# Performance work log

Hardware: AMD Instinct MI355X
Metric: run time of the kernel (lower is better)

Reference implementation:

```python
import jax, jax.numpy as jnp
import numpy as np

B, C, E, H = 4, 2048, 1024, 16
D = E // H
EPS = 1e-5

def _layernorm(x, g, b):
    mu = jnp.mean(x, axis=-1, keepdims=True)
    var = jnp.mean(jnp.square(x - mu), axis=-1, keepdims=True)
    return (x - mu) * jax.lax.rsqrt(var + EPS) * g + b

def setup_inputs() -> dict:
    key = jax.random.key(0)
    ks = jax.random.split(key, 12)
    s = 1.0 / np.sqrt(E)
    return {
        "inputs": jax.random.normal(ks[0], (B, C, E), dtype=jnp.float32),
        "Wq": jax.random.normal(ks[1], (E, E), dtype=jnp.float32) * s,
        "bq": jnp.zeros((E,), dtype=jnp.float32),
        "Wk": jax.random.normal(ks[2], (E, E), dtype=jnp.float32) * s,
        "bk": jnp.zeros((E,), dtype=jnp.float32),
        "Wv": jax.random.normal(ks[3], (E, E), dtype=jnp.float32) * s,
        "bv": jnp.zeros((E,), dtype=jnp.float32),
        "g1": jnp.ones((E,), dtype=jnp.float32),
        "beta1": jnp.zeros((E,), dtype=jnp.float32),
        "g2": jnp.ones((E,), dtype=jnp.float32),
        "beta2": jnp.zeros((E,), dtype=jnp.float32),
        "W1": jax.random.normal(ks[4], (E, 4 * E), dtype=jnp.float32) * s,
        "bm1": jnp.zeros((4 * E,), dtype=jnp.float32),
        "W2": jax.random.normal(ks[5], (4 * E, E), dtype=jnp.float32) * (1.0 / np.sqrt(4 * E)),
        "bm2": jnp.zeros((E,), dtype=jnp.float32),
    }

def reference(inputs, Wq, bq, Wk, bk, Wv, bv, g1, beta1, g2, beta2, W1, bm1, W2, bm2):
    b, c, e = inputs.shape
    normed = _layernorm(inputs, g1, beta1)
    q = (normed @ Wq + bq).reshape(b, c, H, D).transpose(0, 2, 1, 3)  # [B,H,C,D]
    k = (normed @ Wk + bk).reshape(b, c, H, D).transpose(0, 2, 1, 3)
    v = (normed @ Wv + bv).reshape(b, c, H, D).transpose(0, 2, 1, 3)
    scores = jnp.einsum('bhqd,bhkd->bhqk', q, k) / np.sqrt(D).astype(np.float32)
    causal = jnp.triu(jnp.ones((c, c), dtype=bool), k=1)  # True above diagonal
    scores = jnp.where(causal, -jnp.inf, scores)
    probs = jax.nn.softmax(scores, axis=-1)
    attn = jnp.einsum('bhqk,bhkd->bhqd', probs, v)
    attn = attn.transpose(0, 2, 1, 3).reshape(b, c, e)
    out = inputs + attn
    h = _layernorm(out, g2, beta2)
    mlp = jax.nn.relu(h @ W1 + bm1) @ W2 + bm2
    return out + mlp
```

## Files before the change

kernel.cpp:

```cpp
#include <hip/hip_runtime.h>
#include <math.h>

#define B_ 4
#define C_ 2048
#define E_ 1024
#define H_ 16
#define D_ 64
#define ROWS_ (B_*C_)

typedef __bf16 bf16x8 __attribute__((ext_vector_type(8)));
typedef float f32x4 __attribute__((ext_vector_type(4)));

__device__ __forceinline__ float b2f(unsigned short u) {
  unsigned int x = ((unsigned int)u) << 16;
  return __builtin_bit_cast(float, x);
}
__device__ __forceinline__ unsigned short f2b(float f) {
  unsigned int x = __builtin_bit_cast(unsigned int, f);
  unsigned int r = (x + 0x7FFFu + ((x >> 16) & 1u)) >> 16;
  return (unsigned short)r;
}
__device__ __forceinline__ unsigned short tob(float f) { return f2b(f); }
__device__ __forceinline__ unsigned short tob(unsigned short u) { return u; }
__device__ __forceinline__ void store_out(float* p, float v) { *p = v; }
__device__ __forceinline__ void store_out(unsigned short* p, float v) { *p = f2b(v); }

__device__ __forceinline__ void async16(const void* g, void* l) {
  __builtin_amdgcn_global_load_lds(
      (__attribute__((address_space(1))) unsigned int*)g,
      (__attribute__((address_space(3))) unsigned int*)l, 16, 0, 0);
}

template <typename InT>
__global__ __launch_bounds__(256) void transpose64(
    const InT* __restrict__ in, unsigned short* __restrict__ out,
    int s_in, int s_out, int Hz, long zs_b, long zs_h, long zs_out)
{
  __shared__ unsigned short t[64][65];
  int z = blockIdx.z;
  long ib = (long)(z / Hz) * zs_b + (long)(z % Hz) * zs_h;
  long ob = (long)z * zs_out;
  int r0 = blockIdx.y * 64, c0 = blockIdx.x * 64;
  int lane = threadIdx.x & 63, grp = threadIdx.x >> 6;
  for (int i = grp; i < 64; i += 4)
    t[i][lane] = tob(in[ib + (long)(r0 + i) * s_in + c0 + lane]);
  __syncthreads();
  for (int i = grp; i < 64; i += 4)
    out[ob + (long)(c0 + i) * s_out + r0 + lane] = t[lane][i];
}

__global__ void concat_bias(const float* __restrict__ q,
                            const float* __restrict__ k,
                            const float* __restrict__ v,
                            float* __restrict__ o)
{
  int i = blockIdx.x * 256 + threadIdx.x;
  o[i] = (i < 1024) ? q[i] : (i < 2048) ? k[i - 1024] : v[i - 2048];
}

__global__ __launch_bounds__(256) void ln_kernel(
    const float* __restrict__ xin, const unsigned short* __restrict__ addend,
    const float* __restrict__ g, const float* __restrict__ beta,
    unsigned short* __restrict__ yout, float* __restrict__ out1)
{
  int row = blockIdx.x, tid = threadIdx.x;
  size_t base = (size_t)row * E_ + tid * 4;
  float4 xa = *(const float4*)(xin + base);
  float v0 = xa.x, v1 = xa.y, v2 = xa.z, v3 = xa.w;
  if (addend) {
    ushort4 aa = *(const ushort4*)(addend + base);
    v0 += b2f(aa.x); v1 += b2f(aa.y); v2 += b2f(aa.z); v3 += b2f(aa.w);
  }
  if (out1) {
    *(float4*)(out1 + base) = make_float4(v0, v1, v2, v3);
  }
  float s = v0 + v1 + v2 + v3;
  float sq = v0*v0 + v1*v1 + v2*v2 + v3*v3;
  #pragma unroll
  for (int off = 32; off >= 1; off >>= 1) {
    s  += __shfl_xor(s, off);
    sq += __shfl_xor(sq, off);
  }
  __shared__ float red[8];
  int wid = tid >> 6;
  if ((tid & 63) == 0) { red[wid] = s; red[4 + wid] = sq; }
  __syncthreads();
  s  = red[0] + red[1] + red[2] + red[3];
  sq = red[4] + red[5] + red[6] + red[7];
  float mu = s * (1.0f / E_);
  float var = sq * (1.0f / E_) - mu * mu;
  float rs = rsqrtf(var + 1e-5f);
  float4 ga = *(const float4*)(g + tid * 4);
  float4 ba = *(const float4*)(beta + tid * 4);
  ushort4 o;
  o.x = f2b((v0 - mu) * rs * ga.x + ba.x);
  o.y = f2b((v1 - mu) * rs * ga.y + ba.y);
  o.z = f2b((v2 - mu) * rs * ga.z + ba.z);
  o.w = f2b((v3 - mu) * rs * ga.w + ba.w);
  *(ushort4*)(yout + base) = o;
}

template <typename OutT>
__global__ __launch_bounds__(256) void gemm_bt(
    const unsigned short* __restrict__ A, const unsigned short* __restrict__ Bt,
    const float* __restrict__ bias, const float* __restrict__ resid,
    OutT* __restrict__ Co, int M, int N, int K, int lda, int ldb,
    int relu, size_t zs)
{
  __shared__ __align__(16) unsigned short As[128 * 64];
  __shared__ __align__(16) unsigned short Bs[128 * 64];
  int tid = threadIdx.x, lane = tid & 63, wid = tid >> 6;
  int lane15 = lane & 15, quad = lane >> 4;

  int i = blockIdx.x;
  int xcd = i & 7, s = i >> 3;
  int bn = s >> 3;
  int bm = xcd * 8 + (s & 7);
  size_t koff = (size_t)blockIdx.z * K;
  Co += (size_t)blockIdx.z * zs;

  int m_lo = (wid & 1) * 64, n_lo = (wid >> 1) * 64;

  f32x4 acc[4][4];
  #pragma unroll
  for (int a = 0; a < 4; ++a)
    #pragma unroll
    for (int bb = 0; bb < 4; ++bb) acc[a][bb] = 0.0f;

  int sr = tid >> 3, sc = tid & 7;
  int scs = (sc ^ (sr & 7)) * 8;
  const unsigned short* Ag = A + koff + (size_t)(bm * 128 + sr) * lda + scs;
  const unsigned short* Bg = Bt + koff + (size_t)(bn * 128 + sr) * ldb + scs;
  unsigned short* Al = &As[wid * 512];
  unsigned short* Bl = &Bs[wid * 512];
  int sw15 = lane15 & 7;

  for (int k0 = 0; k0 < K; k0 += 64) {
    async16(Ag,                     Al);
    async16(Ag + (size_t)32 * lda,  Al + 32 * 64);
    async16(Ag + (size_t)64 * lda,  Al + 64 * 64);
    async16(Ag + (size_t)96 * lda,  Al + 96 * 64);
    async16(Bg,                     Bl);
    async16(Bg + (size_t)32 * ldb,  Bl + 32 * 64);
    async16(Bg + (size_t)64 * ldb,  Bl + 64 * 64);
    async16(Bg + (size_t)96 * ldb,  Bl + 96 * 64);
    Ag += 64; Bg += 64;
    __syncthreads();

    #pragma unroll
    for (int kk = 0; kk < 2; ++kk) {
      bf16x8 af[4], bfr[4];
      int qs = kk * 4 + quad;
      #pragma unroll
      for (int t = 0; t < 4; ++t)
        af[t] = *(const bf16x8*)&As[(m_lo + t * 16 + lane15) * 64 + ((qs ^ sw15) * 8)];
      #pragma unroll
      for (int t = 0; t < 4; ++t)
        bfr[t] = *(const bf16x8*)&Bs[(n_lo + t * 16 + lane15) * 64 + ((qs ^ sw15) * 8)];
      #pragma unroll
      for (int mt = 0; mt < 4; ++mt)
        #pragma unroll
        for (int nt = 0; nt < 4; ++nt)
          acc[mt][nt] = __builtin_amdgcn_mfma_f32_16x16x32_bf16(af[mt], bfr[nt], acc[mt][nt], 0, 0, 0);
    }
    __syncthreads();
  }

  #pragma unroll
  for (int nt = 0; nt < 4; ++nt) {
    int col = bn * 128 + n_lo + nt * 16 + lane15;
    float bv = bias ? bias[col] : 0.0f;
    #pragma unroll
    for (int mt = 0; mt < 4; ++mt) {
      int row0 = bm * 128 + m_lo + mt * 16 + quad * 4;
      #pragma unroll
      for (int r = 0; r < 4; ++r) {
        float val = acc[mt][nt][r] + bv;
        if (relu) val = fmaxf(val, 0.0f);
        if (resid) val += resid[(size_t)(row0 + r) * N + col];
        store_out(&Co[(size_t)(row0 + r) * N + col], val);
      }
    }
  }
}

__global__ __launch_bounds__(256) void combine2(
    const float* __restrict__ p0, const float* __restrict__ p1,
    const float* __restrict__ resid, const float* __restrict__ bias,
    float* __restrict__ out)
{
  int row = blockIdx.x, tid = threadIdx.x;
  size_t base = (size_t)row * E_ + tid * 4;
  float4 a = *(const float4*)(p0 + base);
  float4 b = *(const float4*)(p1 + base);
  float4 r = *(const float4*)(resid + base);
  float4 bi = *(const float4*)(bias + tid * 4);
  float4 o = make_float4(a.x + b.x + r.x + bi.x, a.y + b.y + r.y + bi.y,
                         a.z + b.z + r.z + bi.z, a.w + b.w + r.w + bi.w);
  *(float4*)(out + base) = o;
}

__global__ __launch_bounds__(512) void attn_kernel(
    const unsigned short* __restrict__ qkv, const unsigned short* __restrict__ vt,
    unsigned short* __restrict__ attnb)
{
  __shared__ __align__(16) unsigned short Klds[64 * 64];
  __shared__ __align__(16) unsigned short Vlds[64 * 64];
  __shared__ __align__(16) unsigned short Plds[8][16 * 72];
  int tid = threadIdx.x, lane = tid & 63, widx = tid >> 6;
  int lane15 = lane & 15, quad = lane >> 4;
  int qblk = 15 - blockIdx.x;
  int bh = blockIdx.y;
  int b = bh >> 4, h = bh & 15;
  int q0w = qblk * 128 + widx * 16;

  const float QSCALE = 0.18033688011112042f;
  const unsigned short* qb = qkv + (size_t)(b * C_ + q0w + lane15) * 3072 + h * 64;
  bf16x8 qa0 = *(const bf16x8*)(qb + quad * 8);
  bf16x8 qa1 = *(const bf16x8*)(qb + 32 + quad * 8);
  #pragma unroll
  for (int j = 0; j < 8; ++j) {
    qa0[j] = (__bf16)((float)qa0[j] * QSCALE);
    qa1[j] = (__bf16)((float)qa1[j] * QSCALE);
  }

  float lsum[4];
  f32x4 o[4];
  #pragma unroll
  for (int r = 0; r < 4; ++r) lsum[r] = 0.0f;
  #pragma unroll
  for (int nt = 0; nt < 4; ++nt) o[nt] = 0.0f;

  int sr = tid >> 3, sc = tid & 7, sw = sr & 7;
  const unsigned short* kg = qkv + (size_t)(b * C_ + sr) * 3072 + 1024 + h * 64 + (sc ^ sw) * 8;
  const unsigned short* vg = vt + (size_t)bh * 64 * 2048 + (size_t)sr * 2048 + (sc ^ sw) * 8;
  unsigned short* kl = &Klds[sr * 64 + sc * 8];
  unsigned short* vl = &Vlds[sr * 64 + sc * 8];
  int swr = lane15 & 7;

  int ntiles = 2 * qblk + 2;
  for (int kt = 0; kt < ntiles; ++kt) {
    int k0 = kt * 64;
    async16(kg, kl);
    async16(vg, vl);
    kg += (size_t)64 * 3072;
    vg += 64;
    __syncthreads();

    if (k0 <= q0w + 15) {
      f32x4 s[4];
      #pragma unroll
      for (int g = 0; g < 4; ++g) s[g] = 0.0f;
      #pragma unroll
      for (int g = 0; g < 4; ++g) {
        int row = g * 16 + lane15;
        bf16x8 kf0 = *(const bf16x8*)&Klds[row * 64 + ((quad ^ swr) * 8)];
        bf16x8 kf1 = *(const bf16x8*)&Klds[row * 64 + (((4 + quad) ^ swr) * 8)];
        s[g] = __builtin_amdgcn_mfma_f32_16x16x32_bf16(qa0, kf0, s[g], 0, 0, 0);
        s[g] = __builtin_amdgcn_mfma_f32_16x16x32_bf16(qa1, kf1, s[g], 0, 0, 0);
      }

      if (k0 + 63 > q0w) {
        #pragma unroll
        for (int g = 0; g < 4; ++g)
          #pragma unroll
          for (int r = 0; r < 4; ++r)
            if (k0 + g * 16 + lane15 > q0w + quad * 4 + r) s[g][r] = -3.0e38f;
      }

      float p[4][4];
      #pragma unroll
      for (int g = 0; g < 4; ++g)
        #pragma unroll
        for (int r = 0; r < 4; ++r) p[g][r] = exp2f(s[g][r]);
      #pragma unroll
      for (int r = 0; r < 4; ++r)
        lsum[r] += (p[0][r] + p[1][r]) + (p[2][r] + p[3][r]);

      __bf16* prow = (__bf16*)&Plds[widx][0];
      #pragma unroll
      for (int g = 0; g < 4; ++g)
        #pragma unroll
        for (int r = 0; r < 4; ++r)
          prow[(quad * 4 + r) * 72 + g * 16 + lane15] = (__bf16)p[g][r];
      asm volatile("s_waitcnt lgkmcnt(0)" ::: "memory");
      bf16x8 pa0 = *(const bf16x8*)&Plds[widx][lane15 * 72 + quad * 8];
      bf16x8 pa1 = *(const bf16x8*)&Plds[widx][lane15 * 72 + 32 + quad * 8];

      #pragma unroll
      for (int nt = 0; nt < 4; ++nt) {
        int d = nt * 16 + lane15;
        bf16x8 vf0 = *(const bf16x8*)&Vlds[d * 64 + ((quad ^ swr) * 8)];
        bf16x8 vf1 = *(const bf16x8*)&Vlds[d * 64 + (((4 + quad) ^ swr) * 8)];
        o[nt] = __builtin_amdgcn_mfma_f32_16x16x32_bf16(pa0, vf0, o[nt], 0, 0, 0);
        o[nt] = __builtin_amdgcn_mfma_f32_16x16x32_bf16(pa1, vf1, o[nt], 0, 0, 0);
      }
    }
    __syncthreads();
  }

  #pragma unroll
  for (int off = 1; off <= 8; off <<= 1)
    #pragma unroll
    for (int r = 0; r < 4; ++r)
      lsum[r] += __shfl_xor(lsum[r], off);
  float rl[4];
  #pragma unroll
  for (int r = 0; r < 4; ++r) rl[r] = 1.0f / lsum[r];

  #pragma unroll
  for (int nt = 0; nt < 4; ++nt) {
    #pragma unroll
    for (int r = 0; r < 4; ++r) {
      float val = o[nt][r] * rl[r];
      attnb[(size_t)(b * C_ + q0w + quad * 4 + r) * E_ + h * 64 + nt * 16 + lane15] = f2b(val);
    }
  }
}

extern "C" void kernel_launch(void* const* d_in, const int* in_sizes, int n_in,
                              void* d_out, int out_size, void* d_ws, size_t ws_size,
                              hipStream_t stream)
{
  const float* x   = (const float*)d_in[0];
  const float* Wq  = (const float*)d_in[1];
  const float* bq  = (const float*)d_in[2];
  const float* Wk  = (const float*)d_in[3];
  const float* bk  = (const float*)d_in[4];
  const float* Wv  = (const float*)d_in[5];
  const float* bv  = (const float*)d_in[6];
  const float* g1  = (const float*)d_in[7];
  const float* be1 = (const float*)d_in[8];
  const float* g2  = (const float*)d_in[9];
  const float* be2 = (const float*)d_in[10];
  const float* W1  = (const float*)d_in[11];
  const float* bm1 = (const float*)d_in[12];
  const float* W2  = (const float*)d_in[13];
  const float* bm2 = (const float*)d_in[14];

  char* ws = (char*)d_ws;
  float*          part0 = (float*)(ws + 0);
  unsigned short* norm1 = (unsigned short*)(ws + 0);
  unsigned short* wT    = (unsigned short*)(ws + 16777216);
  unsigned short* w1T   = (unsigned short*)(ws + 23068672);
  float*          biasq = (float*)(ws + 39845888);
  unsigned short* qkv   = (unsigned short*)(ws + 39858176);
  unsigned short* vtb   = (unsigned short*)(ws + 90189824);
  unsigned short* mid   = (unsigned short*)(ws + 39858176);
  unsigned short* attnb = (unsigned short*)(ws + 106967040);
  float*          out1  = (float*)(ws + 123744256);
  unsigned short* w2T   = (unsigned short*)(ws + 157298688);
  float*          part1 = (float*)(ws + 165687296);
  size_t part_zs = ((size_t)165687296) / 4;

  transpose64<float><<<dim3(16, 16, 1), 256, 0, stream>>>(Wq, wT,               1024, 1024, 1, 0, 0, 0);
  transpose64<float><<<dim3(16, 16, 1), 256, 0, stream>>>(Wk, wT + 1024 * 1024, 1024, 1024, 1, 0, 0, 0);
  transpose64<float><<<dim3(16, 16, 1), 256, 0, stream>>>(Wv, wT + 2048 * 1024, 1024, 1024, 1, 0, 0, 0);
  transpose64<float><<<dim3(64, 16, 1), 256, 0, stream>>>(W1, w1T, 4096, 1024, 1, 0, 0, 0);
  transpose64<float><<<dim3(16, 64, 1), 256, 0, stream>>>(W2, w2T, 1024, 4096, 1, 0, 0, 0);
  concat_bias<<<12, 256, 0, stream>>>(bq, bk, bv, biasq);

  ln_kernel<<<ROWS_, 256, 0, stream>>>(x, nullptr, g1, be1, norm1, nullptr);

  gemm_bt<unsigned short><<<dim3(24 * 64, 1, 1), 256, 0, stream>>>(
      norm1, wT, biasq, nullptr, qkv, 8192, 3072, 1024, 1024, 1024, 0, 0);

  transpose64<unsigned short><<<dim3(1, 32, 64), 256, 0, stream>>>(
      qkv + 2048, vtb, 3072, 2048, 16, (long)C_ * 3072, 64, (long)64 * 2048);

  attn_kernel<<<dim3(16, 64), 512, 0, stream>>>(qkv, vtb, attnb);

  ln_kernel<<<ROWS_, 256, 0, stream>>>(x, attnb, g2, be2, norm1, out1);

  gemm_bt<unsigned short><<<dim3(32 * 64, 1, 1), 256, 0, stream>>>(
      norm1, w1T, bm1, nullptr, mid, 8192, 4096, 1024, 1024, 1024, 1, 0);

  gemm_bt<float><<<dim3(8 * 64, 1, 2), 256, 0, stream>>>(
      mid, w2T, nullptr, nullptr, part0, 8192, 1024, 2048, 4096, 4096, 0, part_zs);
  combine2<<<ROWS_, 256, 0, stream>>>(part0, part1, out1, bm2, (float*)d_out);
}
```

Before: 564.1 us.

## Use 32x32 MFMA tiles in attention and fold bias/residual into split-K GEMM

The attention kernel is rewritten to use 32x32x16 bf16 MFMA with 32 query rows per wave and 256-thread blocks instead of 16x16x32 MFMA with 512 threads. Each block now handles 128 queries with fewer waves, which halves redundant K/V LDS reads per query and raises MFMA efficiency. In exchange it uses more registers (16 row sums and two 16-wide accumulators) and zero-fills half-tiles for causal skipping. The second MLP GEMM's first split-K slice now adds the bias and residual, so the final combine kernel only sums the two partials.

```diff
diff --git a/kernel.cpp b/kernel.cpp
--- a/kernel.cpp
+++ b/kernel.cpp
@@ -10,6 +10,7 @@
 
 typedef __bf16 bf16x8 __attribute__((ext_vector_type(8)));
 typedef float f32x4 __attribute__((ext_vector_type(4)));
+typedef float f32x16 __attribute__((ext_vector_type(16)));
 
 __device__ __forceinline__ float b2f(unsigned short u) {
   unsigned int x = ((unsigned int)u) << 16;
@@ -117,6 +118,7 @@
   int bn = s >> 3;
   int bm = xcd * 8 + (s & 7);
   size_t koff = (size_t)blockIdx.z * K;
+  int z0 = (blockIdx.z == 0);
   Co += (size_t)blockIdx.z * zs;
 
   int m_lo = (wid & 1) * 64, n_lo = (wid >> 1) * 64;
@@ -169,7 +171,7 @@
   #pragma unroll
   for (int nt = 0; nt < 4; ++nt) {
     int col = bn * 128 + n_lo + nt * 16 + lane15;
-    float bv = bias ? bias[col] : 0.0f;
+    float bv = (bias && z0) ? bias[col] : 0.0f;
     #pragma unroll
     for (int mt = 0; mt < 4; ++mt) {
       int row0 = bm * 128 + m_lo + mt * 16 + quad * 4;
@@ -177,143 +179,133 @@
       for (int r = 0; r < 4; ++r) {
         float val = acc[mt][nt][r] + bv;
         if (relu) val = fmaxf(val, 0.0f);
-        if (resid) val += resid[(size_t)(row0 + r) * N + col];
+        if (resid && z0) val += resid[(size_t)(row0 + r) * N + col];
         store_out(&Co[(size_t)(row0 + r) * N + col], val);
       }
     }
   }
 }
 
-__global__ __launch_bounds__(256) void combine2(
+__global__ __launch_bounds__(256) void add2(
     const float* __restrict__ p0, const float* __restrict__ p1,
-    const float* __restrict__ resid, const float* __restrict__ bias,
     float* __restrict__ out)
 {
-  int row = blockIdx.x, tid = threadIdx.x;
-  size_t base = (size_t)row * E_ + tid * 4;
-  float4 a = *(const float4*)(p0 + base);
-  float4 b = *(const float4*)(p1 + base);
-  float4 r = *(const float4*)(resid + base);
-  float4 bi = *(const float4*)(bias + tid * 4);
-  float4 o = make_float4(a.x + b.x + r.x + bi.x, a.y + b.y + r.y + bi.y,
-                         a.z + b.z + r.z + bi.z, a.w + b.w + r.w + bi.w);
-  *(float4*)(out + base) = o;
-}
-
-__global__ __launch_bounds__(512) void attn_kernel(
+  size_t i = ((size_t)blockIdx.x * 256 + threadIdx.x) * 4;
+  float4 a = *(const float4*)(p0 + i);
+  float4 b = *(const float4*)(p1 + i);
+  *(float4*)(out + i) = make_float4(a.x + b.x, a.y + b.y, a.z + b.z, a.w + b.w);
+}
+
+__global__ __launch_bounds__(256) void attn_kernel(
     const unsigned short* __restrict__ qkv, const unsigned short* __restrict__ vt,
     unsigned short* __restrict__ attnb)
 {
   __shared__ __align__(16) unsigned short Klds[64 * 64];
   __shared__ __align__(16) unsigned short Vlds[64 * 64];
-  __shared__ __align__(16) unsigned short Plds[8][16 * 72];
+  __shared__ __align__(16) unsigned short Plds[4][32 * 64];
   int tid = threadIdx.x, lane = tid & 63, widx = tid >> 6;
-  int lane15 = lane & 15, quad = lane >> 4;
+  int lane31 = lane & 31, half = lane >> 5;
   int qblk = 15 - blockIdx.x;
   int bh = blockIdx.y;
   int b = bh >> 4, h = bh & 15;
-  int q0w = qblk * 128 + widx * 16;
+  int q0w = qblk * 128 + widx * 32;
+  int swr = lane31 & 7;
 
   const float QSCALE = 0.18033688011112042f;
-  const unsigned short* qb = qkv + (size_t)(b * C_ + q0w + lane15) * 3072 + h * 64;
-  bf16x8 qa0 = *(const bf16x8*)(qb + quad * 8);
-  bf16x8 qa1 = *(const bf16x8*)(qb + 32 + quad * 8);
-  #pragma unroll
-  for (int j = 0; j < 8; ++j) {
-    qa0[j] = (__bf16)((float)qa0[j] * QSCALE);
-    qa1[j] = (__bf16)((float)qa1[j] * QSCALE);
-  }
-
-  float lsum[4];
-  f32x4 o[4];
-  #pragma unroll
-  for (int r = 0; r < 4; ++r) lsum[r] = 0.0f;
-  #pragma unroll
-  for (int nt = 0; nt < 4; ++nt) o[nt] = 0.0f;
-
-  int sr = tid >> 3, sc = tid & 7, sw = sr & 7;
-  const unsigned short* kg = qkv + (size_t)(b * C_ + sr) * 3072 + 1024 + h * 64 + (sc ^ sw) * 8;
-  const unsigned short* vg = vt + (size_t)bh * 64 * 2048 + (size_t)sr * 2048 + (sc ^ sw) * 8;
+  const unsigned short* qb = qkv + (size_t)(b * C_ + q0w + lane31) * 3072 + h * 64 + half * 8;
+  bf16x8 qa[4];
+  #pragma unroll
+  for (int kk = 0; kk < 4; ++kk) {
+    qa[kk] = *(const bf16x8*)(qb + kk * 16);
+    #pragma unroll
+    for (int j = 0; j < 8; ++j) qa[kk][j] = (__bf16)((float)qa[kk][j] * QSCALE);
+  }
+
+  float lsum[16];
+  f32x16 o[2];
+  #pragma unroll
+  for (int r = 0; r < 16; ++r) lsum[r] = 0.0f;
+  o[0] = 0.0f; o[1] = 0.0f;
+
+  int sr = tid >> 3, sc = tid & 7;
+  int scs = (sc ^ (sr & 7)) * 8;
+  const unsigned short* kg = qkv + (size_t)(b * C_ + sr) * 3072 + 1024 + h * 64 + scs;
+  const unsigned short* vg = vt + (size_t)bh * 64 * 2048 + (size_t)sr * 2048 + scs;
   unsigned short* kl = &Klds[sr * 64 + sc * 8];
   unsigned short* vl = &Vlds[sr * 64 + sc * 8];
-  int swr = lane15 & 7;
+  __bf16* prow = (__bf16*)&Plds[widx][0];
 
   int ntiles = 2 * qblk + 2;
   for (int kt = 0; kt < ntiles; ++kt) {
     int k0 = kt * 64;
-    async16(kg, kl);
-    async16(vg, vl);
+    async16(kg,                      kl);
+    async16(kg + (size_t)32 * 3072,  kl + 32 * 64);
+    async16(vg,                      vl);
+    async16(vg + 32 * 2048,          vl + 32 * 64);
     kg += (size_t)64 * 3072;
     vg += 64;
     __syncthreads();
 
-    if (k0 <= q0w + 15) {
-      f32x4 s[4];
-      #pragma unroll
-      for (int g = 0; g < 4; ++g) s[g] = 0.0f;
-      #pragma unroll
-      for (int g = 0; g < 4; ++g) {
-        int row = g * 16 + lane15;
-        bf16x8 kf0 = *(const bf16x8*)&Klds[row * 64 + ((quad ^ swr) * 8)];
-        bf16x8 kf1 = *(const bf16x8*)&Klds[row * 64 + (((4 + quad) ^ swr) * 8)];
-        s[g] = __builtin_amdgcn_mfma_f32_16x16x32_bf16(qa0, kf0, s[g], 0, 0, 0);
-        s[g] = __builtin_amdgcn_mfma_f32_16x16x32_bf16(qa1, kf1, s[g], 0, 0, 0);
+    if (k0 <= q0w + 31) {
+      #pragma unroll
+      for (int t = 0; t < 2; ++t) {
+        int n0 = t * 32;
+        int keyb = k0 + n0;
+        if (keyb <= q0w + 31) {
+          f32x16 s; s = 0.0f;
+          #pragma unroll
+          for (int kk = 0; kk < 4; ++kk) {
+            bf16x8 kf = *(const bf16x8*)&Klds[(n0 + lane31) * 64 + (((kk * 2 + half) ^ swr) * 8)];
+            s = __builtin_amdgcn_mfma_f32_32x32x16_bf16(qa[kk], kf, s, 0, 0, 0);
+          }
+          int needmask = (keyb + 31 > q0w);
+          #pragma unroll
+          for (int reg = 0; reg < 16; ++reg) {
+            int rowl = (reg & 3) + 8 * (reg >> 2) + 4 * half;
+            float sv = s[reg];
+            if (needmask && (keyb + lane31 > q0w + rowl)) sv = -3.0e38f;
+            float pv = exp2f(sv);
+            lsum[reg] += pv;
+            prow[rowl * 64 + ((((n0 + lane31) >> 3) ^ (rowl & 7)) * 8) + (lane31 & 7)] = (__bf16)pv;
+          }
+        } else {
+          #pragma unroll
+          for (int reg = 0; reg < 16; ++reg) {
+            int rowl = (reg & 3) + 8 * (reg >> 2) + 4 * half;
+            prow[rowl * 64 + ((((n0 + lane31) >> 3) ^ (rowl & 7)) * 8) + (lane31 & 7)] = (__bf16)0.0f;
+          }
+        }
       }
-
-      if (k0 + 63 > q0w) {
+      asm volatile("s_waitcnt lgkmcnt(0)" ::: "memory");
+      bf16x8 pa[4];
+      #pragma unroll
+      for (int kk = 0; kk < 4; ++kk)
+        pa[kk] = *(const bf16x8*)&Plds[widx][lane31 * 64 + (((kk * 2 + half) ^ swr) * 8)];
+      #pragma unroll
+      for (int nt = 0; nt < 2; ++nt) {
         #pragma unroll
-        for (int g = 0; g < 4; ++g)
-          #pragma unroll
-          for (int r = 0; r < 4; ++r)
-            if (k0 + g * 16 + lane15 > q0w + quad * 4 + r) s[g][r] = -3.0e38f;
-      }
-
-      float p[4][4];
-      #pragma unroll
-      for (int g = 0; g < 4; ++g)
-        #pragma unroll
-        for (int r = 0; r < 4; ++r) p[g][r] = exp2f(s[g][r]);
-      #pragma unroll
-      for (int r = 0; r < 4; ++r)
-        lsum[r] += (p[0][r] + p[1][r]) + (p[2][r] + p[3][r]);
-
-      __bf16* prow = (__bf16*)&Plds[widx][0];
-      #pragma unroll
-      for (int g = 0; g < 4; ++g)
-        #pragma unroll
-        for (int r = 0; r < 4; ++r)
-          prow[(quad * 4 + r) * 72 + g * 16 + lane15] = (__bf16)p[g][r];
-      asm volatile("s_waitcnt lgkmcnt(0)" ::: "memory");
-      bf16x8 pa0 = *(const bf16x8*)&Plds[widx][lane15 * 72 + quad * 8];
-      bf16x8 pa1 = *(const bf16x8*)&Plds[widx][lane15 * 72 + 32 + quad * 8];
-
-      #pragma unroll
-      for (int nt = 0; nt < 4; ++nt) {
-        int d = nt * 16 + lane15;
-        bf16x8 vf0 = *(const bf16x8*)&Vlds[d * 64 + ((quad ^ swr) * 8)];
-        bf16x8 vf1 = *(const bf16x8*)&Vlds[d * 64 + (((4 + quad) ^ swr) * 8)];
-        o[nt] = __builtin_amdgcn_mfma_f32_16x16x32_bf16(pa0, vf0, o[nt], 0, 0, 0);
-        o[nt] = __builtin_amdgcn_mfma_f32_16x16x32_bf16(pa1, vf1, o[nt], 0, 0, 0);
+        for (int kk = 0; kk < 4; ++kk) {
+          bf16x8 vf = *(const bf16x8*)&Vlds[(nt * 32 + lane31) * 64 + (((kk * 2 + half) ^ swr) * 8)];
+          o[nt] = __builtin_amdgcn_mfma_f32_32x32x16_bf16(pa[kk], vf, o[nt], 0, 0, 0);
+        }
       }
     }
     __syncthreads();
   }
 
   #pragma unroll
-  for (int off = 1; off <= 8; off <<= 1)
-    #pragma unroll
-    for (int r = 0; r < 4; ++r)
-      lsum[r] += __shfl_xor(lsum[r], off);
-  float rl[4];
-  #pragma unroll
-  for (int r = 0; r < 4; ++r) rl[r] = 1.0f / lsum[r];
-
-  #pragma unroll
-  for (int nt = 0; nt < 4; ++nt) {
-    #pragma unroll
-    for (int r = 0; r < 4; ++r) {
-      float val = o[nt][r] * rl[r];
-      attnb[(size_t)(b * C_ + q0w + quad * 4 + r) * E_ + h * 64 + nt * 16 + lane15] = f2b(val);
+  for (int off = 1; off <= 16; off <<= 1)
+    #pragma unroll
+    for (int reg = 0; reg < 16; ++reg)
+      lsum[reg] += __shfl_xor(lsum[reg], off);
+
+  #pragma unroll
+  for (int nt = 0; nt < 2; ++nt) {
+    #pragma unroll
+    for (int reg = 0; reg < 16; ++reg) {
+      int rowl = (reg & 3) + 8 * (reg >> 2) + 4 * half;
+      float val = o[nt][reg] / lsum[reg];
+      attnb[(size_t)(b * C_ + q0w + rowl) * E_ + h * 64 + nt * 32 + lane31] = f2b(val);
     }
   }
 }
@@ -368,7 +360,7 @@
   transpose64<unsigned short><<<dim3(1, 32, 64), 256, 0, stream>>>(
       qkv + 2048, vtb, 3072, 2048, 16, (long)C_ * 3072, 64, (long)64 * 2048);
 
-  attn_kernel<<<dim3(16, 64), 512, 0, stream>>>(qkv, vtb, attnb);
+  attn_kernel<<<dim3(16, 64), 256, 0, stream>>>(qkv, vtb, attnb);
 
   ln_kernel<<<ROWS_, 256, 0, stream>>>(x, attnb, g2, be2, norm1, out1);
 
@@ -376,6 +368,6 @@
       norm1, w1T, bm1, nullptr, mid, 8192, 4096, 1024, 1024, 1024, 1, 0);
 
   gemm_bt<float><<<dim3(8 * 64, 1, 2), 256, 0, stream>>>(
-      mid, w2T, nullptr, nullptr, part0, 8192, 1024, 2048, 4096, 4096, 0, part_zs);
-  combine2<<<ROWS_, 256, 0, stream>>>(part0, part1, out1, bm2, (float*)d_out);
-}
+      mid, w2T, bm2, out1, part0, 8192, 1024, 2048, 4096, 4096, 0, part_zs);
+  add2<<<8192, 256, 0, stream>>>(part0, part1, (float*)d_out);
+}
```

New measurement: 614.4 us. 8.9% more time.

## Split long causal attention blocks across two workgroups and fold bias/residual into GEMM

Applied to the files above, without the earlier changes.

The eight longest query blocks per head now have their key range split between two workgroups, which write unnormalized partial outputs and row sums to fp32 scratch. A new combine kernel sums the halves and normalizes them. This evens out the triangular causal workload and raises the number of workgroups from 1024 to 1536. Separately, bias and residual for the second MLP GEMM are added in the z=0 split epilogue, leaving a simpler two-input add kernel. In exchange it adds an extra launch and scratch traffic, and relies on the absence of a running max staying safe when the halves are summed.

```diff
diff --git a/kernel.cpp b/kernel.cpp
--- a/kernel.cpp
+++ b/kernel.cpp
@@ -117,6 +117,7 @@
   int bn = s >> 3;
   int bm = xcd * 8 + (s & 7);
   size_t koff = (size_t)blockIdx.z * K;
+  int z0 = (blockIdx.z == 0);
   Co += (size_t)blockIdx.z * zs;
 
   int m_lo = (wid & 1) * 64, n_lo = (wid >> 1) * 64;
@@ -169,7 +170,7 @@
   #pragma unroll
   for (int nt = 0; nt < 4; ++nt) {
     int col = bn * 128 + n_lo + nt * 16 + lane15;
-    float bv = bias ? bias[col] : 0.0f;
+    float bv = (bias && z0) ? bias[col] : 0.0f;
     #pragma unroll
     for (int mt = 0; mt < 4; ++mt) {
       int row0 = bm * 128 + m_lo + mt * 16 + quad * 4;
@@ -177,39 +178,43 @@
       for (int r = 0; r < 4; ++r) {
         float val = acc[mt][nt][r] + bv;
         if (relu) val = fmaxf(val, 0.0f);
-        if (resid) val += resid[(size_t)(row0 + r) * N + col];
+        if (resid && z0) val += resid[(size_t)(row0 + r) * N + col];
         store_out(&Co[(size_t)(row0 + r) * N + col], val);
       }
     }
   }
 }
 
-__global__ __launch_bounds__(256) void combine2(
+__global__ __launch_bounds__(256) void add2(
     const float* __restrict__ p0, const float* __restrict__ p1,
-    const float* __restrict__ resid, const float* __restrict__ bias,
     float* __restrict__ out)
 {
-  int row = blockIdx.x, tid = threadIdx.x;
-  size_t base = (size_t)row * E_ + tid * 4;
-  float4 a = *(const float4*)(p0 + base);
-  float4 b = *(const float4*)(p1 + base);
-  float4 r = *(const float4*)(resid + base);
-  float4 bi = *(const float4*)(bias + tid * 4);
-  float4 o = make_float4(a.x + b.x + r.x + bi.x, a.y + b.y + r.y + bi.y,
-                         a.z + b.z + r.z + bi.z, a.w + b.w + r.w + bi.w);
-  *(float4*)(out + base) = o;
+  size_t i = ((size_t)blockIdx.x * 256 + threadIdx.x) * 4;
+  float4 a = *(const float4*)(p0 + i);
+  float4 b = *(const float4*)(p1 + i);
+  *(float4*)(out + i) = make_float4(a.x + b.x, a.y + b.y, a.z + b.z, a.w + b.w);
 }
 
 __global__ __launch_bounds__(512) void attn_kernel(
     const unsigned short* __restrict__ qkv, const unsigned short* __restrict__ vt,
-    unsigned short* __restrict__ attnb)
+    unsigned short* __restrict__ attnb,
+    float* __restrict__ opart0, float* __restrict__ opart1,
+    float* __restrict__ lpart)
 {
   __shared__ __align__(16) unsigned short Klds[64 * 64];
   __shared__ __align__(16) unsigned short Vlds[64 * 64];
   __shared__ __align__(16) unsigned short Plds[8][16 * 72];
   int tid = threadIdx.x, lane = tid & 63, widx = tid >> 6;
   int lane15 = lane & 15, quad = lane >> 4;
-  int qblk = 15 - blockIdx.x;
+
+  int bx = blockIdx.x;
+  int qblk, p, split;
+  if (bx < 16) { qblk = 15 - (bx >> 1); p = bx & 1; split = 1; }
+  else         { qblk = 23 - bx;        p = 0;      split = 0; }
+  int ntiles = 2 * qblk + 2;
+  int kt0 = (split && p) ? (qblk + 1) : 0;
+  int kt1 = (split && !p) ? (qblk + 1) : ntiles;
+
   int bh = blockIdx.y;
   int b = bh >> 4, h = bh & 15;
   int q0w = qblk * 128 + widx * 16;
@@ -232,14 +237,13 @@
   for (int nt = 0; nt < 4; ++nt) o[nt] = 0.0f;
 
   int sr = tid >> 3, sc = tid & 7, sw = sr & 7;
-  const unsigned short* kg = qkv + (size_t)(b * C_ + sr) * 3072 + 1024 + h * 64 + (sc ^ sw) * 8;
-  const unsigned short* vg = vt + (size_t)bh * 64 * 2048 + (size_t)sr * 2048 + (sc ^ sw) * 8;
+  const unsigned short* kg = qkv + (size_t)(b * C_ + kt0 * 64 + sr) * 3072 + 1024 + h * 64 + (sc ^ sw) * 8;
+  const unsigned short* vg = vt + (size_t)bh * 64 * 2048 + (size_t)sr * 2048 + (sc ^ sw) * 8 + kt0 * 64;
   unsigned short* kl = &Klds[sr * 64 + sc * 8];
   unsigned short* vl = &Vlds[sr * 64 + sc * 8];
   int swr = lane15 & 7;
 
-  int ntiles = 2 * qblk + 2;
-  for (int kt = 0; kt < ntiles; ++kt) {
+  for (int kt = kt0; kt < kt1; ++kt) {
     int k0 = kt * 64;
     async16(kg, kl);
     async16(vg, vl);
@@ -268,21 +272,21 @@
             if (k0 + g * 16 + lane15 > q0w + quad * 4 + r) s[g][r] = -3.0e38f;
       }
 
-      float p[4][4];
+      float pv[4][4];
       #pragma unroll
       for (int g = 0; g < 4; ++g)
         #pragma unroll
-        for (int r = 0; r < 4; ++r) p[g][r] = exp2f(s[g][r]);
+        for (int r = 0; r < 4; ++r) pv[g][r] = exp2f(s[g][r]);
       #pragma unroll
       for (int r = 0; r < 4; ++r)
-        lsum[r] += (p[0][r] + p[1][r]) + (p[2][r] + p[3][r]);
+        lsum[r] += (pv[0][r] + pv[1][r]) + (pv[2][r] + pv[3][r]);
 
       __bf16* prow = (__bf16*)&Plds[widx][0];
       #pragma unroll
       for (int g = 0; g < 4; ++g)
         #pragma unroll
         for (int r = 0; r < 4; ++r)
-          prow[(quad * 4 + r) * 72 + g * 16 + lane15] = (__bf16)p[g][r];
+          prow[(quad * 4 + r) * 72 + g * 16 + lane15] = (__bf16)pv[g][r];
       asm volatile("s_waitcnt lgkmcnt(0)" ::: "memory");
       bf16x8 pa0 = *(const bf16x8*)&Plds[widx][lane15 * 72 + quad * 8];
       bf16x8 pa1 = *(const bf16x8*)&Plds[widx][lane15 * 72 + 32 + quad * 8];
@@ -304,18 +308,46 @@
     #pragma unroll
     for (int r = 0; r < 4; ++r)
       lsum[r] += __shfl_xor(lsum[r], off);
-  float rl[4];
-  #pragma unroll
-  for (int r = 0; r < 4; ++r) rl[r] = 1.0f / lsum[r];
-
-  #pragma unroll
-  for (int nt = 0; nt < 4; ++nt) {
-    #pragma unroll
-    for (int r = 0; r < 4; ++r) {
-      float val = o[nt][r] * rl[r];
-      attnb[(size_t)(b * C_ + q0w + quad * 4 + r) * E_ + h * 64 + nt * 16 + lane15] = f2b(val);
+
+  if (!split) {
+    float rl[4];
+    #pragma unroll
+    for (int r = 0; r < 4; ++r) rl[r] = 1.0f / lsum[r];
+    #pragma unroll
+    for (int nt = 0; nt < 4; ++nt)
+      #pragma unroll
+      for (int r = 0; r < 4; ++r) {
+        float val = o[nt][r] * rl[r];
+        attnb[(size_t)(b * C_ + q0w + quad * 4 + r) * E_ + h * 64 + nt * 16 + lane15] = f2b(val);
+      }
+  } else {
+    float* op = p ? opart1 : opart0;
+    size_t rbase = (size_t)bh * 1024 + (q0w - 1024) + quad * 4;
+    #pragma unroll
+    for (int nt = 0; nt < 4; ++nt)
+      #pragma unroll
+      for (int r = 0; r < 4; ++r)
+        op[(rbase + r) * 64 + nt * 16 + lane15] = o[nt][r];
+    if (lane15 == 0) {
+      float* lp = lpart + (size_t)p * 65536;
+      #pragma unroll
+      for (int r = 0; r < 4; ++r) lp[rbase + r] = lsum[r];
     }
   }
+}
+
+__global__ __launch_bounds__(256) void attn_combine(
+    const float* __restrict__ opart0, const float* __restrict__ opart1,
+    const float* __restrict__ lpart, unsigned short* __restrict__ attnb)
+{
+  size_t i = (size_t)blockIdx.x * 256 + threadIdx.x;
+  int d = (int)(i & 63);
+  size_t rowi = i >> 6;
+  int bh = (int)(rowi >> 10), row = (int)(rowi & 1023);
+  float ov = opart0[rowi * 64 + d] + opart1[rowi * 64 + d];
+  float lv = lpart[rowi] + lpart[65536 + rowi];
+  int b = bh >> 4, h = bh & 15;
+  attnb[(size_t)(b * C_ + 1024 + row) * E_ + h * 64 + d] = f2b(ov / lv);
 }
 
 extern "C" void kernel_launch(void* const* d_in, const int* in_sizes, int n_in,
@@ -351,6 +383,9 @@
   float*          out1  = (float*)(ws + 123744256);
   unsigned short* w2T   = (unsigned short*)(ws + 157298688);
   float*          part1 = (float*)(ws + 165687296);
+  float*          opart0 = (float*)(ws + 165687296);
+  float*          opart1 = (float*)(ws + 123744256);
+  float*          lpartb = (float*)(ws + 0);
   size_t part_zs = ((size_t)165687296) / 4;
 
   transpose64<float><<<dim3(16, 16, 1), 256, 0, stream>>>(Wq, wT,               1024, 1024, 1, 0, 0, 0);
@@ -368,7 +403,8 @@
   transpose64<unsigned short><<<dim3(1, 32, 64), 256, 0, stream>>>(
       qkv + 2048, vtb, 3072, 2048, 16, (long)C_ * 3072, 64, (long)64 * 2048);
 
-  attn_kernel<<<dim3(16, 64), 512, 0, stream>>>(qkv, vtb, attnb);
+  attn_kernel<<<dim3(24, 64), 512, 0, stream>>>(qkv, vtb, attnb, opart0, opart1, lpartb);
+  attn_combine<<<16384, 256, 0, stream>>>(opart0, opart1, lpartb, attnb);
 
   ln_kernel<<<ROWS_, 256, 0, stream>>>(x, attnb, g2, be2, norm1, out1);
 
@@ -376,6 +412,6 @@
       norm1, w1T, bm1, nullptr, mid, 8192, 4096, 1024, 1024, 1024, 1, 0);
 
   gemm_bt<float><<<dim3(8 * 64, 1, 2), 256, 0, stream>>>(
-      mid, w2T, nullptr, nullptr, part0, 8192, 1024, 2048, 4096, 4096, 0, part_zs);
-  combine2<<<ROWS_, 256, 0, stream>>>(part0, part1, out1, bm2, (float*)d_out);
-}
+      mid, w2T, bm2, out1, part0, 8192, 1024, 2048, 4096, 4096, 0, part_zs);
+  add2<<<8192, 256, 0, stream>>>(part0, part1, (float*)d_out);
+}
```

Measured after the change: 553.0 us. -2.0%, faster.
